# Optimization experiments

Measured on AMD Instinct MI355X. Metric: run time of the kernel, lower is better.

The kernel has to match this reference:

```python
import jax, jax.numpy as jnp
import numpy as np

B, P_H, P_W, D, M, IMG = 8, 28, 28, 128, 30000, 224


def setup_inputs() -> dict:
    key = jax.random.key(0)
    k1, k2 = jax.random.split(key)
    features = jax.random.normal(k1, (B * P_H * P_W, D), dtype=jnp.float32)
    memory_bank = jax.random.normal(k2, (M, D), dtype=jnp.float32)
    return {
        "features": features,
        "memory_bank": memory_bank,
        "batchsize": B,
        "scale_h": P_H,
        "scale_w": P_W,
        "image_size": IMG,
    }


def reference(features, memory_bank, batchsize, scale_h, scale_w, image_size):
    # FAISS IndexFlatL2 1-NN: squared L2 distance to nearest memory-bank entry.
    # ||f - m||^2 = ||f||^2 + ||m||^2 - 2 f.m   (single GEMM, then row-min)
    f2 = jnp.sum(features * features, axis=1, keepdims=True)            # [N,1]
    m2 = jnp.sum(memory_bank * memory_bank, axis=1)                     # [M]
    dists = f2 + m2[None, :] - 2.0 * (features @ memory_bank.T)         # [N,M]
    nn_dist = jnp.min(dists, axis=1)                                     # [N]; k=1 so mean over k is identity
    patch_scores = nn_dist.reshape(batchsize, scale_h, scale_w)
    image_scores = jnp.max(patch_scores.reshape(batchsize, -1), axis=1)  # [B]
    # F.interpolate(mode='bilinear', align_corners=False) == half-pixel bilinear resize
    up = jax.image.resize(
        patch_scores[:, None, :, :],
        (batchsize, 1, image_size, image_size),
        method="bilinear",
    )[:, 0]                                                               # [B, IMG, IMG]
    return image_scores, up
```

## Files before the change

kernel.cpp:

```cpp
#include <hip/hip_runtime.h>
#include <hip/hip_bf16.h>
#include <math.h>

#define N_FEAT 6272
#define DIM    128
#define M_BANK 30000
#define M_PAD  30080
#define NB     8
#define PH     28
#define PW     28
#define IMG    224
#define BM     256
#define BN     128
#define TPT    5
#define CHUNKS 47
#define TILE_BYTES 16384

#define BANKQ_BLOCKS (M_PAD / 64)
#define FEATQ_BLOCKS (N_FEAT / 64)

typedef __attribute__((ext_vector_type(4)))  int    i32x4;
typedef __attribute__((ext_vector_type(8)))  int    i32x8;
typedef __attribute__((ext_vector_type(4)))  float  f32x4;
typedef __attribute__((ext_vector_type(2)))  float  f32x2;

typedef const __attribute__((address_space(1))) unsigned int g_u32;
typedef __attribute__((address_space(3))) unsigned int l_u32;

static __device__ __forceinline__ void q32(const float* x, i32x4& q0, i32x4& q1) {
    #pragma unroll
    for (int d = 0; d < 4; ++d) {
        int t = __builtin_amdgcn_cvt_pk_fp8_f32(x[d*4+0], x[d*4+1], 0, false);
        t     = __builtin_amdgcn_cvt_pk_fp8_f32(x[d*4+2], x[d*4+3], t, true);
        q0[d] = t;
    }
    #pragma unroll
    for (int d = 0; d < 4; ++d) {
        int t = __builtin_amdgcn_cvt_pk_fp8_f32(x[16+d*4+0], x[16+d*4+1], 0, false);
        t     = __builtin_amdgcn_cvt_pk_fp8_f32(x[16+d*4+2], x[16+d*4+3], t, true);
        q1[d] = t;
    }
}

__global__ __launch_bounds__(256) void prep_all(const float* __restrict__ bank,
                                                const float* __restrict__ feat,
                                                unsigned char* __restrict__ mbq,
                                                unsigned char* __restrict__ fbq,
                                                float* __restrict__ m2h,
                                                unsigned long long* __restrict__ nn64) {
    const int tid = threadIdx.x;
    const int c   = tid >> 2;
    const int s   = tid & 3;
    float x[32];
    if (blockIdx.x < BANKQ_BLOCKS) {
        const int r = blockIdx.x * 64 + c;
        const bool valid = r < M_BANK;
        if (valid) {
            #pragma unroll
            for (int i = 0; i < 8; ++i) {
                f32x4 v = *(const f32x4*)(bank + (size_t)r * DIM + s * 32 + i * 4);
                x[i*4+0]=v.x; x[i*4+1]=v.y; x[i*4+2]=v.z; x[i*4+3]=v.w;
            }
        } else {
            #pragma unroll
            for (int i = 0; i < 32; ++i) x[i] = 0.f;
        }
        float sum = 0.f;
        #pragma unroll
        for (int i = 0; i < 32; ++i) sum += x[i] * x[i];
        sum += __shfl_xor(sum, 1);
        sum += __shfl_xor(sum, 2);
        i32x4 q0, q1;
        q32(x, q0, q1);
        unsigned char* base = mbq + (size_t)(r >> 7) * TILE_BYTES + s * 4096 + (r & 127) * 16;
        *(i32x4*)(base)        = q0;
        *(i32x4*)(base + 2048) = q1;
        if (s == 0) m2h[r] = valid ? (-0.5f * (sum + 1024.0f)) : -1e30f;
        return;
    }
    const int r = (blockIdx.x - BANKQ_BLOCKS) * 64 + c;
    #pragma unroll
    for (int i = 0; i < 8; ++i) {
        f32x4 v = *(const f32x4*)(feat + (size_t)r * DIM + s * 32 + i * 4);
        x[i*4+0]=v.x; x[i*4+1]=v.y; x[i*4+2]=v.z; x[i*4+3]=v.w;
    }
    i32x4 q0, q1;
    q32(x, q0, q1);
    *(i32x4*)(fbq + (size_t)r * DIM + s * 32)      = q0;
    *(i32x4*)(fbq + (size_t)r * DIM + s * 32 + 16) = q1;
    if (s == 0) nn64[r] = 0xFFFFFFFFFFFFFFFFull;
}

__global__ __launch_bounds__(256, 3) void dist_min_kernel(
        const unsigned char* __restrict__ fbq, const unsigned char* __restrict__ mbq,
        const float* __restrict__ m2h, unsigned long long* __restrict__ nn64) {
    __shared__ __align__(16) unsigned char lds[2 * TILE_BYTES];
    const int tid  = threadIdx.x;
    const int lane = tid & 63;
    const int w    = tid >> 6;
    const int c16  = lane & 15;
    const int kq   = lane >> 4;
    const int arow = blockIdx.x * BM + w * 64;
    const int tile0 = blockIdx.y * TPT;

    i32x8 afrag[4];
    #pragma unroll
    for (int mb = 0; mb < 4; ++mb) {
        int row = arow + mb * 16 + c16;
        if (row >= N_FEAT) row = N_FEAT - 1;
        ((i32x4*)&afrag[mb])[0] = *(const i32x4*)(fbq + (size_t)row * DIM + kq * 32);
        ((i32x4*)&afrag[mb])[1] = *(const i32x4*)(fbq + (size_t)row * DIM + kq * 32 + 16);
    }

    float maxp[4][4];
    #pragma unroll
    for (int mb = 0; mb < 4; ++mb)
        #pragma unroll
        for (int j = 0; j < 4; ++j) maxp[mb][j] = -INFINITY;

#define STAGE(tile_idx, bufsel)                                                      \
    {   const unsigned char* sp_ = mbq + (size_t)(tile_idx) * TILE_BYTES + tid * 16; \
        unsigned char* dp_ = lds + (bufsel) * TILE_BYTES + tid * 16;                 \
        _Pragma("unroll")                                                            \
        for (int i_ = 0; i_ < 4; ++i_)                                               \
            __builtin_amdgcn_global_load_lds((g_u32*)(sp_ + i_ * 4096),              \
                                             (l_u32*)(dp_ + i_ * 4096), 16, 0, 0); }

    float m2c[8];
    #pragma unroll
    for (int n = 0; n < 8; ++n) m2c[n] = m2h[tile0 * BN + n * 16 + c16];
    STAGE(tile0, 0);
    __syncthreads();

    int cur = 0;
    #pragma unroll 1
    for (int t = 0; t < TPT; ++t) {
        float m2n[8];
        if (t + 1 < TPT) {
            #pragma unroll
            for (int n = 0; n < 8; ++n)
                m2n[n] = m2h[(tile0 + t + 1) * BN + n * 16 + c16];
            STAGE(tile0 + t + 1, cur ^ 1);
        }
        const unsigned char* buf = lds + cur * TILE_BYTES;
        #pragma unroll 4
        for (int n = 0; n < 8; ++n) {
            const int col = n * 16 + c16;
            i32x8 bfrag;
            ((i32x4*)&bfrag)[0] = *(const i32x4*)(buf + kq * 4096 + col * 16);
            ((i32x4*)&bfrag)[1] = *(const i32x4*)(buf + kq * 4096 + 2048 + col * 16);
            const f32x4 cin = {m2c[n], m2c[n], m2c[n], m2c[n]};
            const unsigned int code = (unsigned int)(((t * 8 + n) << 4) | c16);
            f32x4 acc[4];
            __builtin_amdgcn_s_setprio(1);
            #pragma unroll
            for (int mb = 0; mb < 4; ++mb)
                acc[mb] = __builtin_amdgcn_mfma_scale_f32_16x16x128_f8f6f4(
                    afrag[mb], bfrag, cin, 0, 0, 0, 127, 0, 127);
            __builtin_amdgcn_s_setprio(0);
            #pragma unroll
            for (int mb = 0; mb < 4; ++mb)
                #pragma unroll
                for (int j = 0; j < 4; ++j) {
                    unsigned int p = (__float_as_uint(acc[mb][j]) & 0xFFFFFC00u) | code;
                    maxp[mb][j] = fmaxf(maxp[mb][j], __uint_as_float(p));
                }
        }
        __syncthreads();
        if (t + 1 < TPT) {
            #pragma unroll
            for (int n = 0; n < 8; ++n) m2c[n] = m2n[n];
        }
        cur ^= 1;
    }
#undef STAGE

    #pragma unroll
    for (int mb = 0; mb < 4; ++mb)
        #pragma unroll
        for (int j = 0; j < 4; ++j) {
            float v = maxp[mb][j];
            v = fmaxf(v, __shfl_xor(v, 1));
            v = fmaxf(v, __shfl_xor(v, 2));
            v = fmaxf(v, __shfl_xor(v, 4));
            v = fmaxf(v, __shfl_xor(v, 8));
            if (c16 == 0) {
                int row = arow + mb * 16 + kq * 4 + j;
                if (row < N_FEAT) {
                    unsigned int bits = __float_as_uint(v);
                    unsigned int code = bits & 1023u;
                    unsigned int tn = code >> 4;
                    unsigned int col = (unsigned int)(tile0 + (tn >> 3)) * BN
                                       + (tn & 7u) * 16 + (code & 15u);
                    unsigned long long pack =
                        ((unsigned long long)__float_as_uint(-v) << 32) | col;
                    atomicMin(nn64 + row, pack);
                }
            }
        }
}

__global__ __launch_bounds__(256) void rescue_kernel(const float* __restrict__ feat,
                                                     const float* __restrict__ bank,
                                                     const unsigned long long* __restrict__ nn64,
                                                     float* __restrict__ nnf) {
    const int row  = blockIdx.x * 4 + (threadIdx.x >> 6);
    const int lane = threadIdx.x & 63;
    const unsigned int idx = (unsigned int)(nn64[row] & 0xFFFFFFFFull);
    f32x2 f = *(const f32x2*)(feat + (size_t)row * DIM + lane * 2);
    f32x2 m = *(const f32x2*)(bank + (size_t)idx * DIM + lane * 2);
    float dx = f.x - m.x, dy = f.y - m.y;
    float d = dx * dx + dy * dy;
    #pragma unroll
    for (int k = 1; k < 64; k <<= 1) d += __shfl_xor(d, k);
    if (lane == 0) nnf[row] = d;
}

#define UP_BLOCKS ((NB * IMG * IMG) / 256)
__global__ __launch_bounds__(256) void finalize_kernel(const float* __restrict__ nnf,
                                                       float* __restrict__ out_scores,
                                                       float* __restrict__ out_up) {
    if (blockIdx.x >= UP_BLOCKS) {
        __shared__ float wmax[4];
        int b = blockIdx.x - UP_BLOCKS;
        int tid = threadIdx.x;
        float v = -INFINITY;
        for (int i = tid; i < PH * PW; i += 256)
            v = fmaxf(v, nnf[b * PH * PW + i]);
        #pragma unroll
        for (int m = 1; m < 64; m <<= 1) v = fmaxf(v, __shfl_xor(v, m));
        if ((tid & 63) == 0) wmax[tid >> 6] = v;
        __syncthreads();
        if (tid == 0)
            out_scores[b] = fmaxf(fmaxf(wmax[0], wmax[1]), fmaxf(wmax[2], wmax[3]));
        return;
    }
    int idx = blockIdx.x * 256 + threadIdx.x;
    int b = idx / (IMG * IMG);
    int rem = idx - b * (IMG * IMG);
    int y = rem / IMG;
    int x = rem - y * IMG;
    float sy = y * 0.125f - 0.4375f;
    float sx = x * 0.125f - 0.4375f;
    float fy = floorf(sy), fx = floorf(sx);
    float ty = sy - fy, tx = sx - fx;
    int y0 = (int)fy, x0 = (int)fx;
    int y1 = min(y0 + 1, PH - 1), x1 = min(x0 + 1, PW - 1);
    y0 = max(y0, 0); x0 = max(x0, 0);
    const float* p = nnf + b * PH * PW;
    float v00 = p[y0 * PW + x0];
    float v01 = p[y0 * PW + x1];
    float v10 = p[y1 * PW + x0];
    float v11 = p[y1 * PW + x1];
    float v0 = v00 + tx * (v01 - v00);
    float v1 = v10 + tx * (v11 - v10);
    out_up[idx] = v0 + ty * (v1 - v0);
}

extern "C" void kernel_launch(void* const* d_in, const int* in_sizes, int n_in,
                              void* d_out, int out_size, void* d_ws, size_t ws_size,
                              hipStream_t stream) {
    const float* feat = (const float*)d_in[0];
    const float* bank = (const float*)d_in[1];
    char* ws = (char*)d_ws;
    unsigned char*      mbq  = (unsigned char*)(ws + 0);
    unsigned char*      fbq  = (unsigned char*)(ws + 3850240);
    float*              m2h  = (float*)(ws + 4653056);
    unsigned long long* nn64 = (unsigned long long*)(ws + 4773376);
    float*              nnf  = (float*)(ws + 4823552);
    float* out_scores = (float*)d_out;
    float* out_up     = out_scores + NB;

    hipLaunchKernelGGL(prep_all, dim3(BANKQ_BLOCKS + FEATQ_BLOCKS), dim3(256), 0, stream,
                       bank, feat, mbq, fbq, m2h, nn64);
    hipLaunchKernelGGL(dist_min_kernel, dim3((N_FEAT + BM - 1) / BM, CHUNKS), dim3(256), 0,
                       stream, fbq, mbq, m2h, nn64);
    hipLaunchKernelGGL(rescue_kernel, dim3(N_FEAT / 4), dim3(256), 0, stream,
                       feat, bank, nn64, nnf);
    hipLaunchKernelGGL(finalize_kernel, dim3(UP_BLOCKS + NB), dim3(256), 0, stream,
                       nnf, out_scores, out_up);
}
```

Before: 51.74 us.

## Replace double-buffered multi-tile loop with single 320-column tile per block

Each block now loads one 320-column quantized bank tile (40 KB) into LDS once and processes it, replacing the 5-tile double-buffered loop over 128-column tiles. The bank quantization layout is changed to match the new tile width, and the occupancy hint goes from 3 to 4 blocks per CU. The aim is to drop per-tile syncs and pipeline bookkeeping and to rely on more resident blocks to hide load latency. The trade-off is that there is no overlap within a block, more blocks are launched, each block has a longer exposed load, and there are more atomicMin writes per row.

New measurement: 58.58 us. 1.13x slower.

```diff
diff --git a/kernel.cpp b/kernel.cpp
--- a/kernel.cpp
+++ b/kernel.cpp
@@ -11,10 +11,9 @@
 #define PW     28
 #define IMG    224
 #define BM     256
-#define BN     128
-#define TPT    5
-#define CHUNKS 47
-#define TILE_BYTES 16384
+#define BN     320
+#define CHUNKS 94
+#define TILE_BYTES 40960
 
 #define BANKQ_BLOCKS (M_PAD / 64)
 #define FEATQ_BLOCKS (N_FEAT / 64)
@@ -72,9 +71,11 @@
         sum += __shfl_xor(sum, 2);
         i32x4 q0, q1;
         q32(x, q0, q1);
-        unsigned char* base = mbq + (size_t)(r >> 7) * TILE_BYTES + s * 4096 + (r & 127) * 16;
+        const int tt  = r / BN;
+        const int col = r - tt * BN;
+        unsigned char* base = mbq + (size_t)tt * TILE_BYTES + s * 10240 + col * 16;
         *(i32x4*)(base)        = q0;
-        *(i32x4*)(base + 2048) = q1;
+        *(i32x4*)(base + 5120) = q1;
         if (s == 0) m2h[r] = valid ? (-0.5f * (sum + 1024.0f)) : -1e30f;
         return;
     }
@@ -91,17 +92,26 @@
     if (s == 0) nn64[r] = 0xFFFFFFFFFFFFFFFFull;
 }
 
-__global__ __launch_bounds__(256, 3) void dist_min_kernel(
+__global__ __launch_bounds__(256, 4) void dist_min_kernel(
         const unsigned char* __restrict__ fbq, const unsigned char* __restrict__ mbq,
         const float* __restrict__ m2h, unsigned long long* __restrict__ nn64) {
-    __shared__ __align__(16) unsigned char lds[2 * TILE_BYTES];
+    __shared__ __align__(16) unsigned char lds[TILE_BYTES];
     const int tid  = threadIdx.x;
     const int lane = tid & 63;
     const int w    = tid >> 6;
     const int c16  = lane & 15;
     const int kq   = lane >> 4;
     const int arow = blockIdx.x * BM + w * 64;
-    const int tile0 = blockIdx.y * TPT;
+    const int tile = blockIdx.y;
+
+    {
+        const unsigned char* sp = mbq + (size_t)tile * TILE_BYTES + tid * 16;
+        unsigned char* dp = lds + tid * 16;
+        #pragma unroll
+        for (int i = 0; i < 10; ++i)
+            __builtin_amdgcn_global_load_lds((g_u32*)(sp + i * 4096),
+                                             (l_u32*)(dp + i * 4096), 16, 0, 0);
+    }
 
     i32x8 afrag[4];
     #pragma unroll
@@ -118,62 +128,34 @@
         #pragma unroll
         for (int j = 0; j < 4; ++j) maxp[mb][j] = -INFINITY;
 
-#define STAGE(tile_idx, bufsel)                                                      \
-    {   const unsigned char* sp_ = mbq + (size_t)(tile_idx) * TILE_BYTES + tid * 16; \
-        unsigned char* dp_ = lds + (bufsel) * TILE_BYTES + tid * 16;                 \
-        _Pragma("unroll")                                                            \
-        for (int i_ = 0; i_ < 4; ++i_)                                               \
-            __builtin_amdgcn_global_load_lds((g_u32*)(sp_ + i_ * 4096),              \
-                                             (l_u32*)(dp_ + i_ * 4096), 16, 0, 0); }
-
-    float m2c[8];
-    #pragma unroll
-    for (int n = 0; n < 8; ++n) m2c[n] = m2h[tile0 * BN + n * 16 + c16];
-    STAGE(tile0, 0);
     __syncthreads();
 
-    int cur = 0;
-    #pragma unroll 1
-    for (int t = 0; t < TPT; ++t) {
-        float m2n[8];
-        if (t + 1 < TPT) {
+    const unsigned char* bufq = lds + kq * 10240;
+    const float* m2p = m2h + tile * BN + c16;
+    #pragma unroll 4
+    for (int n = 0; n < 20; ++n) {
+        const int col = n * 16 + c16;
+        i32x8 bfrag;
+        ((i32x4*)&bfrag)[0] = *(const i32x4*)(bufq + col * 16);
+        ((i32x4*)&bfrag)[1] = *(const i32x4*)(bufq + 5120 + col * 16);
+        const float m2c = m2p[n * 16];
+        const f32x4 cin = {m2c, m2c, m2c, m2c};
+        const unsigned int code = (unsigned int)((n << 4) | c16);
+        f32x4 acc[4];
+        __builtin_amdgcn_s_setprio(1);
+        #pragma unroll
+        for (int mb = 0; mb < 4; ++mb)
+            acc[mb] = __builtin_amdgcn_mfma_scale_f32_16x16x128_f8f6f4(
+                afrag[mb], bfrag, cin, 0, 0, 0, 127, 0, 127);
+        __builtin_amdgcn_s_setprio(0);
+        #pragma unroll
+        for (int mb = 0; mb < 4; ++mb)
             #pragma unroll
-            for (int n = 0; n < 8; ++n)
-                m2n[n] = m2h[(tile0 + t + 1) * BN + n * 16 + c16];
-            STAGE(tile0 + t + 1, cur ^ 1);
-        }
-        const unsigned char* buf = lds + cur * TILE_BYTES;
-        #pragma unroll 4
-        for (int n = 0; n < 8; ++n) {
-            const int col = n * 16 + c16;
-            i32x8 bfrag;
-            ((i32x4*)&bfrag)[0] = *(const i32x4*)(buf + kq * 4096 + col * 16);
-            ((i32x4*)&bfrag)[1] = *(const i32x4*)(buf + kq * 4096 + 2048 + col * 16);
-            const f32x4 cin = {m2c[n], m2c[n], m2c[n], m2c[n]};
-            const unsigned int code = (unsigned int)(((t * 8 + n) << 4) | c16);
-            f32x4 acc[4];
-            __builtin_amdgcn_s_setprio(1);
-            #pragma unroll
-            for (int mb = 0; mb < 4; ++mb)
-                acc[mb] = __builtin_amdgcn_mfma_scale_f32_16x16x128_f8f6f4(
-                    afrag[mb], bfrag, cin, 0, 0, 0, 127, 0, 127);
-            __builtin_amdgcn_s_setprio(0);
-            #pragma unroll
-            for (int mb = 0; mb < 4; ++mb)
-                #pragma unroll
-                for (int j = 0; j < 4; ++j) {
-                    unsigned int p = (__float_as_uint(acc[mb][j]) & 0xFFFFFC00u) | code;
-                    maxp[mb][j] = fmaxf(maxp[mb][j], __uint_as_float(p));
-                }
-        }
-        __syncthreads();
-        if (t + 1 < TPT) {
-            #pragma unroll
-            for (int n = 0; n < 8; ++n) m2c[n] = m2n[n];
-        }
-        cur ^= 1;
-    }
-#undef STAGE
+            for (int j = 0; j < 4; ++j) {
+                unsigned int p = (__float_as_uint(acc[mb][j]) & 0xFFFFFC00u) | code;
+                maxp[mb][j] = fmaxf(maxp[mb][j], __uint_as_float(p));
+            }
+    }
 
     #pragma unroll
     for (int mb = 0; mb < 4; ++mb)
@@ -189,9 +171,8 @@
                 if (row < N_FEAT) {
                     unsigned int bits = __float_as_uint(v);
                     unsigned int code = bits & 1023u;
-                    unsigned int tn = code >> 4;
-                    unsigned int col = (unsigned int)(tile0 + (tn >> 3)) * BN
-                                       + (tn & 7u) * 16 + (code & 15u);
+                    unsigned int col = (unsigned int)tile * BN
+                                       + (code >> 4) * 16 + (code & 15u);
                     unsigned long long pack =
                         ((unsigned long long)__float_as_uint(-v) << 32) | col;
                     atomicMin(nn64 + row, pack);
```
